# Kernel tuning notes

Measured on AMD Instinct MI355X. Metric: run time of the kernel, lower is better.

The kernel has to match this reference:

```python
import jax, jax.numpy as jnp
import numpy as np

L, N, C, OPL = 20, 512, 10, 13        # levels, nodes/level, conditions/node, condition op length
HID, MID = 512, 256                   # hidden_dim, hid_dim
OP_DIM, EX_DIM, SAMP_DIM = 15, 108, 1000
EPS = 1e-5


def _lstm_cell(x, h, c, wih, whh, bih, bhh):
    gates = x @ wih.T + h @ whh.T + bih + bhh
    i, f, g, o = jnp.split(gates, 4, axis=-1)  # torch gate order i,f,g,o
    c = jax.nn.sigmoid(f) * c + jax.nn.sigmoid(i) * jnp.tanh(g)
    h = jax.nn.sigmoid(o) * jnp.tanh(c)
    return h, c


def _batchnorm(x, g, b):  # training-mode BatchNorm1d (biased batch stats)
    m = x.mean(0)
    v = x.var(0)
    return (x - m) / jnp.sqrt(v + EPS) * g + b


def setup_inputs() -> dict:
    key = jax.random.key(0)
    ks = iter(jax.random.split(key, 48))
    rn = lambda shp, s=1.0: jax.random.normal(next(ks), shp, jnp.float32) * s
    ru = lambda shp: jax.random.uniform(next(ks), shp, jnp.float32)
    w = lambda shp: rn(shp, 0.05)
    inp = {
        'operators': ru((L, N, OP_DIM)),
        'extra_infos': rn((L, N, EX_DIM)),
        'condition1s': rn((L, N, C, OPL)),
        'condition2s': rn((L, N, C, OPL)),
        'samples': ru((L, N, SAMP_DIM)),
        'condition_masks': jnp.ones((L, N, 1), jnp.float32),
        'mapping': jax.random.randint(next(ks), (L, 2, N), 0, N + 1),
        # lstm1 (condition encoder)
        'w_ih1': w((4 * HID, OPL)), 'w_hh1': w((4 * HID, HID)),
        'b_ih1': w((4 * HID,)), 'b_hh1': w((4 * HID,)),
        # mlps feeding the tree lstm
        'sample_w': w((MID, SAMP_DIM)), 'sample_b': w((MID,)),
        'cond_w': w((MID, HID)), 'cond_b': w((MID,)),
        'bn1_g': jnp.ones((MID,), jnp.float32), 'bn1_b': jnp.zeros((MID,), jnp.float32),
        # lstm2 (tree aggregation)
        'w_ih2': w((4 * HID, OP_DIM + EX_DIM + 2 * MID)), 'w_hh2': w((4 * HID, HID)),
        'b_ih2': w((4 * HID,)), 'b_hh2': w((4 * HID,)),
        'bn2_g': jnp.ones((HID,), jnp.float32), 'bn2_b': jnp.zeros((HID,), jnp.float32),
        # task heads
        't1_w2': w((MID, HID)), 't1_b2': w((MID,)),
        't2_w2': w((MID, HID)), 't2_b2': w((MID,)),
        'bn3_g': jnp.ones((MID,), jnp.float32), 'bn3_b': jnp.zeros((MID,), jnp.float32),
        't1_w3': w((MID, MID)), 't1_b3': w((MID,)),
        't2_w3': w((MID, MID)), 't2_b3': w((MID,)),
        't1_ow': w((1, MID)), 't1_ob': w((1,)),
        't2_ow': w((1, MID)), 't2_ob': w((1,)),
    }
    return inp


def reference(operators, extra_infos, condition1s, condition2s, samples, condition_masks, mapping,
              w_ih1, w_hh1, b_ih1, b_hh1, sample_w, sample_b, cond_w, cond_b, bn1_g, bn1_b,
              w_ih2, w_hh2, b_ih2, b_hh2, bn2_g, bn2_b,
              t1_w2, t1_b2, t2_w2, t2_b2, bn3_g, bn3_b,
              t1_w3, t1_b3, t2_w3, t2_b3, t1_ow, t1_ob, t2_ow, t2_ob):
    Lv, Np = operators.shape[0], operators.shape[1]
    mapping = mapping.astype(jnp.int32)

    # --- condition encoder: lstm1 over each node's predicate sequence ---
    x = condition1s.reshape(Lv * Np, C, OPL)
    h0 = jnp.zeros((Lv * Np, HID), operators.dtype)

    def step1(carry, xt):
        h, c = carry
        h, c = _lstm_cell(xt, h, c, w_ih1, w_hh1, b_ih1, b_hh1)
        return (h, c), None

    (h_last, _), _ = jax.lax.scan(step1, (h0, h0), jnp.swapaxes(x, 0, 1))
    cond = _batchnorm(jax.nn.relu(h_last @ cond_w.T + cond_b), bn1_g, bn1_b)
    cond = cond.reshape(Lv, Np, MID)

    samp = jax.nn.relu(samples @ sample_w.T + sample_b) * condition_masks
    feats = jnp.concatenate([operators, extra_infos, cond, samp], axis=2)  # [L, N, 123+2*MID]

    # --- bottom level: lstm2 single step from zero state ---
    z0 = jnp.zeros((Np, HID), feats.dtype)
    hid, cid = _lstm_cell(feats[Lv - 1], z0, z0, w_ih2, w_hh2, b_ih2, b_hh2)

    # --- bottom-up tree aggregation: gather children states, average, lstm2 step ---
    def level_step(carry, inputs):
        hid, cid = carry
        x_lvl, mapp = inputs  # x_lvl [N, F], mapp [2, N], index 0 == pad (no child)
        pad = jnp.zeros((1, HID), hid.dtype)
        nh = jnp.concatenate([pad, hid], axis=0)  # [N+1, H]
        nc = jnp.concatenate([pad, cid], axis=0)
        h = (nh[mapp[0]] + nh[mapp[1]]) * 0.5
        c = (nc[mapp[0]] + nc[mapp[1]]) * 0.5
        hid, cid = _lstm_cell(x_lvl, h, c, w_ih2, w_hh2, b_ih2, b_hh2)
        return (hid, cid), None

    xs = (feats[Lv - 2::-1], mapping[Lv - 2::-1])
    (hid, cid), _ = jax.lax.scan(level_step, (hid, cid), xs)

    # --- heads (batch_size == Np: all level-0 nodes active for these inputs) ---
    z = _batchnorm(hid, bn2_g, bn2_b)
    t1 = _batchnorm(jax.nn.relu(z @ t1_w2.T + t1_b2), bn3_g, bn3_b)
    t1 = jax.nn.sigmoid(jax.nn.relu(t1 @ t1_w3.T + t1_b3) @ t1_ow.T + t1_ob)
    t2 = _batchnorm(jax.nn.relu(z @ t2_w2.T + t2_b2), bn3_g, bn3_b)
    t2 = jax.nn.sigmoid(jax.nn.relu(t2 @ t2_w3.T + t2_b3) @ t2_ow.T + t2_ob)
    return t1, t2
```

## Files before the change

kernel.cpp:

```cpp
#include <hip/hip_runtime.h>
#include <hip/hip_bf16.h>


typedef __bf16 bf16x8 __attribute__((ext_vector_type(8)));
typedef float f32x4 __attribute__((ext_vector_type(4)));

#define MROWS 10240
#define LDH1  552
#define L1_ROWS 48
#define L1_BLOCKS 214
#define SAMP_BASE 214
#define FEAT_BASE 374
#define FUSED_BLOCKS 414

#define PF_BIAS1   0
#define PF_BIAS2   2048
#define PF_CONDB   4096
#define PF_SAMPB   4352
#define PF_BCAT2   4608
#define PF_B3CAT   5120
#define PF_BN1G    5632
#define PF_BN1B    5888
#define PF_BN2G    6144
#define PF_BN2B    6656
#define PF_BN3G    7168
#define PF_BN3B    7424
#define PF_OW      7680
#define PF_OB      8192
#define PF_TOTAL   8194

__device__ __forceinline__ float fsig(float x) {
  return __builtin_amdgcn_rcpf(1.0f + __expf(-x));
}
__device__ __forceinline__ float ftanh(float x) {
  return fmaf(2.0f, __builtin_amdgcn_rcpf(1.0f + __expf(-2.0f * x)), -1.0f);
}
__device__ __forceinline__ bf16x8 bzero8() {
  bf16x8 z;
#pragma unroll
  for (int i = 0; i < 8; ++i) z[i] = (__bf16)0.0f;
  return z;
}
__device__ __forceinline__ float ld_in(const void* p, long i, int bf) {
  return bf ? (float)((const __bf16*)p)[i] : ((const float*)p)[i];
}

__global__ void detect_kernel(const unsigned* __restrict__ masks, int* __restrict__ flag) {
  if (blockIdx.x == 0 && threadIdx.x == 0)
    *flag = (masks[0] == 0x3F803F80u) ? 1 : 0;
}

__global__ void prep_kernel(const int* __restrict__ flagp,
    const void* w_ih1, const void* w_hh1, const void* b_ih1, const void* b_hh1,
    const void* w_ih2, const void* w_hh2, const void* b_ih2, const void* b_hh2,
    const void* t1_w2, const void* t2_w2, const void* t1_b2, const void* t2_b2,
    const void* cond_w, const void* cond_b, const void* sample_w, const void* sample_b,
    const void* bn1_g, const void* bn1_b, const void* bn2_g, const void* bn2_b,
    const void* bn3_g, const void* bn3_b,
    const void* t1_w3, const void* t1_b3, const void* t2_w3, const void* t2_b3,
    const void* t1_ow, const void* t1_ob, const void* t2_ow, const void* t2_ob,
    const void* masks,
    __bf16* __restrict__ w1s, __bf16* __restrict__ w2s,
    __bf16* __restrict__ wcat2, __bf16* __restrict__ cond_w_bf,
    __bf16* __restrict__ sample_w_bf, __bf16* __restrict__ w3cat_bf,
    float* __restrict__ mask_f, float* __restrict__ pf)
{
  const int bf = *flagp;
  const int S1 = 2048 * 544;
  const int S2 = 2048 * 1152;
  const int S3 = 512 * 512;
  const int S4 = 256 * 512;
  const int S5 = 256 * 1000;
  const int S6 = 512 * 256;
  const int S7 = 10240;
  const int total = S1 + S2 + S3 + S4 + S5 + S6 + S7 + PF_TOTAL;
  for (int idx = blockIdx.x * blockDim.x + threadIdx.x; idx < total;
       idx += gridDim.x * blockDim.x) {
    int i = idx;
    if (i < S1) {
      int e = i & 7, l = (i >> 3) & 63, g = (i >> 9) & 3;
      int grp = i >> 11;
      int kk = grp % 17, cgt = grp / 17;
      int colq = l & 15, quad = l >> 4;
      int row = g * 512 + cgt * 16 + colq;
      int k = kk * 32 + quad * 8 + e;
      float v = (k < 512) ? ld_in(w_hh1, (long)row * 512 + k, bf)
              : (k < 525) ? ld_in(w_ih1, (long)row * 13 + (k - 512), bf) : 0.0f;
      w1s[i] = (__bf16)v;
      continue;
    }
    i -= S1;
    if (i < S2) {
      int e = i & 7, l = (i >> 3) & 63, g = (i >> 9) & 3;
      int grp = i >> 11;
      int kk = grp % 36, jt = grp / 36;
      int colq = l & 15, quad = l >> 4;
      int row = g * 512 + jt * 16 + colq;
      int k = kk * 32 + quad * 8 + e;
      float v = (k < 635) ? ld_in(w_ih2, (long)row * 635 + k, bf)
              : (k < 640) ? 0.0f : ld_in(w_hh2, (long)row * 512 + (k - 640), bf);
      w2s[i] = (__bf16)v;
      continue;
    }
    i -= S2;
    if (i < S3) {
      int r = i >> 9, k = i & 511;
      wcat2[i] = (__bf16)((r < 256) ? ld_in(t1_w2, r * 512 + k, bf)
                                    : ld_in(t2_w2, (r - 256) * 512 + k, bf));
      continue;
    }
    i -= S3;
    if (i < S4) { cond_w_bf[i] = (__bf16)ld_in(cond_w, i, bf); continue; }
    i -= S4;
    if (i < S5) { sample_w_bf[i] = (__bf16)ld_in(sample_w, i, bf); continue; }
    i -= S5;
    if (i < S6) {
      int r = i >> 8, k = i & 255;
      w3cat_bf[i] = (__bf16)((r < 256) ? ld_in(t1_w3, r * 256 + k, bf)
                                       : ld_in(t2_w3, (r - 256) * 256 + k, bf));
      continue;
    }
    i -= S6;
    if (i < S7) { mask_f[i] = ld_in(masks, i, bf); continue; }
    i -= S7;
    {
      int j = i;
      float v;
      if      (j < 2048) v = ld_in(b_ih1, j, bf) + ld_in(b_hh1, j, bf);
      else if (j < 4096) v = ld_in(b_ih2, j - 2048, bf) + ld_in(b_hh2, j - 2048, bf);
      else if (j < 4352) v = ld_in(cond_b, j - 4096, bf);
      else if (j < 4608) v = ld_in(sample_b, j - 4352, bf);
      else if (j < 5120) { int k = j - 4608; v = (k < 256) ? ld_in(t1_b2, k, bf) : ld_in(t2_b2, k - 256, bf); }
      else if (j < 5632) { int k = j - 5120; v = (k < 256) ? ld_in(t1_b3, k, bf) : ld_in(t2_b3, k - 256, bf); }
      else if (j < 5888) v = ld_in(bn1_g, j - 5632, bf);
      else if (j < 6144) v = ld_in(bn1_b, j - 5888, bf);
      else if (j < 6656) v = ld_in(bn2_g, j - 6144, bf);
      else if (j < 7168) v = ld_in(bn2_b, j - 6656, bf);
      else if (j < 7424) v = ld_in(bn3_g, j - 7168, bf);
      else if (j < 7680) v = ld_in(bn3_b, j - 7424, bf);
      else if (j < 8192) { int k = j - 7680; v = (k < 256) ? ld_in(t1_ow, k, bf) : ld_in(t2_ow, k - 256, bf); }
      else v = (j == 8192) ? ld_in(t1_ob, 0, bf) : ld_in(t2_ob, 0, bf);
      pf[j] = v;
    }
  }
}

__global__ void conv_samples_kernel(const int* __restrict__ flagp,
                                    const void* __restrict__ samples,
                                    __bf16* __restrict__ dst)
{
  const int bf = *flagp;
  if (bf) return;
  for (long i = blockIdx.x * blockDim.x + threadIdx.x; i < 10240000L;
       i += (long)gridDim.x * blockDim.x)
    dst[i] = (__bf16)ld_in(samples, i, bf);
}

__global__ __launch_bounds__(1024, 4) void fused1_kernel(
    const int* __restrict__ flagp,
    const void* __restrict__ cond1,
    const __bf16* __restrict__ w1s,
    const float*  __restrict__ bias,
    __bf16* __restrict__ h_out,
    const void* __restrict__ samples_raw,
    const __bf16* __restrict__ samp_bf,
    const __bf16* __restrict__ sample_w_bf,
    const float* __restrict__ sampb,
    __bf16* __restrict__ samp_out,
    const float* __restrict__ mask,
    const void* __restrict__ ops,
    const void* __restrict__ extra,
    __bf16* __restrict__ Astage,
    const __bf16* __restrict__ cond_w_bf,
    const float* __restrict__ condb,
    float* __restrict__ condtmp,
    float* __restrict__ partial)
{
  const int bf = *flagp;
  const int tid = threadIdx.x;

  if (blockIdx.x < L1_BLOCKS) {
    __shared__ __attribute__((aligned(16))) __bf16 hbuf[2][L1_ROWS * LDH1];
    const int wave = tid >> 6;
    const int lane = tid & 63;
    const int colq = lane & 15;
    const int quad = lane >> 4;
    const int r0   = blockIdx.x * L1_ROWS;

    {
      bf16x8 z8 = bzero8();
      for (int i = tid * 8; i < 2 * L1_ROWS * LDH1; i += 1024 * 8)
        *(bf16x8*)&hbuf[0][i] = z8;
    }
    __syncthreads();
    if (tid < L1_ROWS * 8) {
      int row = tid >> 3, jj = tid & 7;
      int gr = r0 + row;
      if (gr < MROWS) {
        long base = (long)gr * 130;
        hbuf[0][row * LDH1 + 512 + jj] = (__bf16)ld_in(cond1, base + jj, bf);
        if (jj < 5) hbuf[0][row * LDH1 + 520 + jj] = (__bf16)ld_in(cond1, base + 8 + jj, bf);
      }
    }
    __syncthreads();

    float c_reg[2][3][4];
#pragma unroll
    for (int a = 0; a < 2; ++a)
#pragma unroll
      for (int b = 0; b < 3; ++b)
#pragma unroll
        for (int r = 0; r < 4; ++r) c_reg[a][b][r] = 0.0f;

    const int jbase = wave * 32;

    float bI[2], bF[2], bG[2], bO[2];
#pragma unroll
    for (int cg = 0; cg < 2; ++cg) {
      const int j = jbase + cg * 16 + colq;
      bI[cg] = bias[j];
      bF[cg] = bias[512 + j];
      bG[cg] = bias[1024 + j];
      bO[cg] = bias[1536 + j];
    }

#pragma unroll 1
    for (int t = 0; t < 10; ++t) {
      const __bf16* hcur = hbuf[t & 1];
      __bf16* hnxt = hbuf[(t + 1) & 1];
#pragma unroll
      for (int cg = 0; cg < 2; ++cg) {
        const int jc = jbase + cg * 16;
        f32x4 acc[3][4];
#pragma unroll
        for (int a = 0; a < 3; ++a)
#pragma unroll
          for (int g = 0; g < 4; ++g)
#pragma unroll
            for (int r = 0; r < 4; ++r) acc[a][g][r] = 0.0f;

        const __bf16* wp = w1s + ((size_t)(wave * 2 + cg) * 17 * 4 * 512) + (lane << 3);
#pragma unroll 1
        for (int kk = 0; kk < 17; ++kk) {
          const int kof = (kk << 5) + (quad << 3);
          bf16x8 af[3];
#pragma unroll
          for (int rt = 0; rt < 3; ++rt)
            af[rt] = *(const bf16x8*)&hcur[(rt * 16 + colq) * LDH1 + kof];
          bf16x8 bfr[4];
#pragma unroll
          for (int g = 0; g < 4; ++g)
            bfr[g] = *(const bf16x8*)&wp[(kk * 4 + g) << 9];
#pragma unroll
          for (int g = 0; g < 4; ++g)
#pragma unroll
            for (int rt = 0; rt < 3; ++rt)
              acc[rt][g] = __builtin_amdgcn_mfma_f32_16x16x32_bf16(af[rt], bfr[g], acc[rt][g], 0, 0, 0);
        }
#pragma unroll
        for (int rt = 0; rt < 3; ++rt)
#pragma unroll
          for (int r = 0; r < 4; ++r) {
            float c = fsig(acc[rt][1][r] + bF[cg]) * c_reg[cg][rt][r]
                    + fsig(acc[rt][0][r] + bI[cg]) * ftanh(acc[rt][2][r] + bG[cg]);
            c_reg[cg][rt][r] = c;
            float h = fsig(acc[rt][3][r] + bO[cg]) * ftanh(c);
            hnxt[(rt * 16 + quad * 4 + r) * LDH1 + jc + colq] = (__bf16)h;
          }
      }
      if (t < 9 && tid < L1_ROWS * 8) {
        int row = tid >> 3, jj = tid & 7;
        int gr = r0 + row;
        if (gr < MROWS) {
          long base = ((long)gr * 10 + (t + 1)) * 13;
          hnxt[row * LDH1 + 512 + jj] = (__bf16)ld_in(cond1, base + jj, bf);
          if (jj < 5) hnxt[row * LDH1 + 520 + jj] = (__bf16)ld_in(cond1, base + 8 + jj, bf);
        }
      }
      __syncthreads();
    }

    for (int i = tid; i < L1_ROWS * 64; i += 1024) {
      int row = i >> 6;
      int cb  = (i & 63) << 3;
      *(bf16x8*)&h_out[(size_t)(r0 + row) * 512 + cb] = *(const bf16x8*)&hbuf[0][row * LDH1 + cb];
    }

    {
      const int ct = wave;
      f32x4 cacc[3];
#pragma unroll
      for (int rt = 0; rt < 3; ++rt)
#pragma unroll
        for (int r = 0; r < 4; ++r) cacc[rt][r] = 0.0f;

      const __bf16* wb = cond_w_bf + (size_t)(ct * 16 + colq) * 512;
#pragma unroll 1
      for (int kk = 0; kk < 16; ++kk) {
        const int kof = (kk << 5) + (quad << 3);
        bf16x8 bfr = *(const bf16x8*)&wb[kof];
#pragma unroll
        for (int rt = 0; rt < 3; ++rt) {
          bf16x8 af = *(const bf16x8*)&hbuf[0][(rt * 16 + colq) * LDH1 + kof];
          cacc[rt] = __builtin_amdgcn_mfma_f32_16x16x32_bf16(af, bfr, cacc[rt], 0, 0, 0);
        }
      }
      const int col = ct * 16 + colq;
      const float bv = condb[col];
      float s1 = 0.0f, s2 = 0.0f;
#pragma unroll
      for (int rt = 0; rt < 3; ++rt)
#pragma unroll
        for (int r = 0; r < 4; ++r) {
          const int lrow = rt * 16 + quad * 4 + r;
          const int grow = r0 + lrow;
          float v = fmaxf(cacc[rt][r] + bv, 0.0f);
          if (grow < MROWS) {
            condtmp[(size_t)grow * 256 + col] = v;
            s1 += v;
            s2 += v * v;
          }
        }
      s1 += __shfl_xor(s1, 16); s2 += __shfl_xor(s2, 16);
      s1 += __shfl_xor(s1, 32); s2 += __shfl_xor(s2, 32);
      if (quad == 0) {
        partial[(size_t)(2 * blockIdx.x) * 256 + col]     = s1;
        partial[(size_t)(2 * blockIdx.x + 1) * 256 + col] = s2;
      }
    }
    return;
  }

  if (blockIdx.x < FEAT_BASE) {
    const __bf16* A = bf ? (const __bf16*)samples_raw : samp_bf;
    const int vb   = (blockIdx.x - SAMP_BASE) * 4 + (tid >> 8);
    const int bx   = vb & 3;
    const int by   = vb >> 2;
    const int t    = tid & 255;
    const int wave = t >> 6;
    const int lane = t & 63;
    const int colq = lane & 15;
    const int quad = lane >> 4;
    const int m0 = by * 64 + (wave >> 1) * 32;
    const int n0 = bx * 64 + (wave & 1) * 32;
    const int K = 1000;

    f32x4 acc[2][2];
#pragma unroll
    for (int a = 0; a < 2; ++a)
#pragma unroll
      for (int b = 0; b < 2; ++b)
#pragma unroll
        for (int r = 0; r < 4; ++r) acc[a][b][r] = 0.0f;

    for (int kk = 0; kk < 32; ++kk) {
      const int kof = (kk << 5) + (quad << 3);
      bf16x8 a0, a1, b0, b1;
      if (kof < K) {
        a0 = *(const bf16x8*)&A[(size_t)(m0 + colq) * 1000 + kof];
        a1 = *(const bf16x8*)&A[(size_t)(m0 + 16 + colq) * 1000 + kof];
        b0 = *(const bf16x8*)&sample_w_bf[(size_t)(n0 + colq) * 1000 + kof];
        b1 = *(const bf16x8*)&sample_w_bf[(size_t)(n0 + 16 + colq) * 1000 + kof];
      } else {
        a0 = bzero8(); a1 = a0; b0 = a0; b1 = a0;
      }
      acc[0][0] = __builtin_amdgcn_mfma_f32_16x16x32_bf16(a0, b0, acc[0][0], 0, 0, 0);
      acc[0][1] = __builtin_amdgcn_mfma_f32_16x16x32_bf16(a0, b1, acc[0][1], 0, 0, 0);
      acc[1][0] = __builtin_amdgcn_mfma_f32_16x16x32_bf16(a1, b0, acc[1][0], 0, 0, 0);
      acc[1][1] = __builtin_amdgcn_mfma_f32_16x16x32_bf16(a1, b1, acc[1][1], 0, 0, 0);
    }
#pragma unroll
    for (int ai = 0; ai < 2; ++ai)
#pragma unroll
      for (int bi = 0; bi < 2; ++bi) {
        const int col = n0 + bi * 16 + colq;
        const float bv = sampb[col];
#pragma unroll
        for (int r = 0; r < 4; ++r) {
          const int row = m0 + ai * 16 + quad * 4 + r;
          float v = fmaxf(acc[ai][bi][r] + bv, 0.0f) * mask[row];
          samp_out[(size_t)row * 640 + col] = (__bf16)v;
        }
      }
    return;
  }

  for (int idx = (blockIdx.x - FEAT_BASE) * 1024 + tid; idx < 10240 * 128;
       idx += 40 * 1024) {
    int m = idx >> 7, c = idx & 127;
    float v; int col;
    if (c < 15)       { v = ld_in(ops, (long)m * 15 + c, bf);            col = c; }
    else if (c < 123) { v = ld_in(extra, (long)m * 108 + (c - 15), bf);  col = c; }
    else              { v = 0.0f;                                        col = 512 + c; }
    Astage[(size_t)m * 640 + col] = (__bf16)v;
  }
}

template<int ACT, int OUTBF, int MASKED>
__global__ __launch_bounds__(256, 4) void gemm_kernel(
    const __bf16* __restrict__ A, int lda,
    const __bf16* __restrict__ W, int ldw,
    const float* __restrict__ bias,
    float* __restrict__ outf, __bf16* __restrict__ outb, int ldc,
    const float* __restrict__ mask, int K)
{
  const int tid  = threadIdx.x;
  const int wave = tid >> 6;
  const int lane = tid & 63;
  const int colq = lane & 15;
  const int quad = lane >> 4;
  const int m0 = blockIdx.y * 64 + (wave >> 1) * 32;
  const int n0 = blockIdx.x * 64 + (wave & 1) * 32;

  f32x4 acc[2][2];
#pragma unroll
  for (int a = 0; a < 2; ++a)
#pragma unroll
    for (int b = 0; b < 2; ++b)
#pragma unroll
      for (int r = 0; r < 4; ++r) acc[a][b][r] = 0.0f;

  const int nk = (K + 31) >> 5;
  for (int kk = 0; kk < nk; ++kk) {
    const int kof = (kk << 5) + (quad << 3);
    bf16x8 a0, a1, b0, b1;
    if (kof < K) {
      a0 = *(const bf16x8*)&A[(size_t)(m0 + colq) * lda + kof];
      a1 = *(const bf16x8*)&A[(size_t)(m0 + 16 + colq) * lda + kof];
      b0 = *(const bf16x8*)&W[(size_t)(n0 + colq) * ldw + kof];
      b1 = *(const bf16x8*)&W[(size_t)(n0 + 16 + colq) * ldw + kof];
    } else {
      a0 = bzero8(); a1 = a0; b0 = a0; b1 = a0;
    }
    acc[0][0] = __builtin_amdgcn_mfma_f32_16x16x32_bf16(a0, b0, acc[0][0], 0, 0, 0);
    acc[0][1] = __builtin_amdgcn_mfma_f32_16x16x32_bf16(a0, b1, acc[0][1], 0, 0, 0);
    acc[1][0] = __builtin_amdgcn_mfma_f32_16x16x32_bf16(a1, b0, acc[1][0], 0, 0, 0);
    acc[1][1] = __builtin_amdgcn_mfma_f32_16x16x32_bf16(a1, b1, acc[1][1], 0, 0, 0);
  }
#pragma unroll
  for (int ai = 0; ai < 2; ++ai)
#pragma unroll
    for (int bi = 0; bi < 2; ++bi) {
      const int col = n0 + bi * 16 + colq;
      const float bv = bias[col];
#pragma unroll
      for (int r = 0; r < 4; ++r) {
        const int row = m0 + ai * 16 + quad * 4 + r;
        float v = acc[ai][bi][r] + bv;
        if (ACT) v = fmaxf(v, 0.0f);
        if (MASKED) v *= mask[row];
        if (OUTBF) outb[(size_t)row * ldc + col] = (__bf16)v;
        else       outf[(size_t)row * ldc + col] = v;
      }
    }
}

__global__ __launch_bounds__(1024, 4) void treelvl_kernel(
    const __bf16* __restrict__ Alvl,
    const __bf16* __restrict__ w2s,
    const float* __restrict__ bias,
    const int* __restrict__ mapping,
    const __bf16* __restrict__ h_src, const float* __restrict__ c_src,
    __bf16* __restrict__ h_dst, float* __restrict__ c_dst,
    float* __restrict__ h_f32, int first, int last)
{
  __shared__ float red[3][16 * 256];
  const int tid  = threadIdx.x;
  const int wave = tid >> 6;
  const int lane = tid & 63;
  const int colq = lane & 15;
  const int quad = lane >> 4;
  const int wv   = wave & 3;
  const int kq   = wave >> 2;
  const int jt = blockIdx.x;
  const int mt = blockIdx.y;
  const int rowA = mt * 64 + wv * 16 + colq;

  const __bf16* wbase = w2s + (size_t)jt * 36 * 4 * 512 + (lane << 3);

  f32x4 acc[4];
#pragma unroll
  for (int g = 0; g < 4; ++g)
#pragma unroll
    for (int r = 0; r < 4; ++r) acc[g][r] = 0.0f;

  if (kq < 2) {
    const __bf16* arow = Alvl + (size_t)rowA * 640;
    const int kb = kq * 10;
#pragma unroll 2
    for (int ki = 0; ki < 10; ++ki) {
      const int kk = kb + ki;
      const int kof = (kk << 5) + (quad << 3);
      bf16x8 afr = *(const bf16x8*)&arow[kof];
      bf16x8 b0 = *(const bf16x8*)&wbase[(kk * 4 + 0) << 9];
      bf16x8 b1 = *(const bf16x8*)&wbase[(kk * 4 + 1) << 9];
      bf16x8 b2 = *(const bf16x8*)&wbase[(kk * 4 + 2) << 9];
      bf16x8 b3 = *(const bf16x8*)&wbase[(kk * 4 + 3) << 9];
      acc[0] = __builtin_amdgcn_mfma_f32_16x16x32_bf16(afr, b0, acc[0], 0, 0, 0);
      acc[1] = __builtin_amdgcn_mfma_f32_16x16x32_bf16(afr, b1, acc[1], 0, 0, 0);
      acc[2] = __builtin_amdgcn_mfma_f32_16x16x32_bf16(afr, b2, acc[2], 0, 0, 0);
      acc[3] = __builtin_amdgcn_mfma_f32_16x16x32_bf16(afr, b3, acc[3], 0, 0, 0);
    }
  } else {
    int i0 = 0, i1 = 0;
    if (!first) { i0 = mapping[rowA]; i1 = mapping[512 + rowA]; }
    const float s0 = (i0 > 0) ? 0.5f : 0.0f;
    const float s1 = (i1 > 0) ? 0.5f : 0.0f;
    const __bf16* h0p = h_src + (size_t)((i0 > 0 ? i0 : 1) - 1) * 512;
    const __bf16* h1p = h_src + (size_t)((i1 > 0 ? i1 : 1) - 1) * 512;
    const int kb = 20 + (kq - 2) * 8;
#pragma unroll 2
    for (int ki = 0; ki < 8; ++ki) {
      const int kk = kb + ki;
      const int kh = ((kk - 20) << 5) + (quad << 3);
      bf16x8 v0 = *(const bf16x8*)&h0p[kh];
      bf16x8 v1 = *(const bf16x8*)&h1p[kh];
      bf16x8 afr;
#pragma unroll
      for (int e = 0; e < 8; ++e)
        afr[e] = (__bf16)((float)v0[e] * s0 + (float)v1[e] * s1);
      bf16x8 b0 = *(const bf16x8*)&wbase[(kk * 4 + 0) << 9];
      bf16x8 b1 = *(const bf16x8*)&wbase[(kk * 4 + 1) << 9];
      bf16x8 b2 = *(const bf16x8*)&wbase[(kk * 4 + 2) << 9];
      bf16x8 b3 = *(const bf16x8*)&wbase[(kk * 4 + 3) << 9];
      acc[0] = __builtin_amdgcn_mfma_f32_16x16x32_bf16(afr, b0, acc[0], 0, 0, 0);
      acc[1] = __builtin_amdgcn_mfma_f32_16x16x32_bf16(afr, b1, acc[1], 0, 0, 0);
      acc[2] = __builtin_amdgcn_mfma_f32_16x16x32_bf16(afr, b2, acc[2], 0, 0, 0);
      acc[3] = __builtin_amdgcn_mfma_f32_16x16x32_bf16(afr, b3, acc[3], 0, 0, 0);
    }
  }

  if (kq > 0) {
    float* rp = red[kq - 1];
    const int base = wv * 64 + lane;
#pragma unroll
    for (int g = 0; g < 4; ++g)
#pragma unroll
      for (int r = 0; r < 4; ++r)
        rp[(g * 4 + r) * 256 + base] = acc[g][r];
  }
  __syncthreads();
  if (kq != 0) return;

  {
    const int base = wv * 64 + lane;
#pragma unroll
    for (int s = 0; s < 3; ++s) {
      const float* rp = red[s];
#pragma unroll
      for (int g = 0; g < 4; ++g)
#pragma unroll
        for (int r = 0; r < 4; ++r)
          acc[g][r] += rp[(g * 4 + r) * 256 + base];
    }
  }

  const int j = jt * 16 + colq;
  const float bi  = bias[j];
  const float bff = bias[512 + j];
  const float bg  = bias[1024 + j];
  const float bo  = bias[1536 + j];
#pragma unroll
  for (int r = 0; r < 4; ++r) {
    const int mrow = mt * 64 + wv * 16 + quad * 4 + r;
    float ci = 0.0f;
    if (!first) {
      int a0 = mapping[mrow], a1 = mapping[512 + mrow];
      if (a0 > 0) ci += c_src[(size_t)(a0 - 1) * 512 + j];
      if (a1 > 0) ci += c_src[(size_t)(a1 - 1) * 512 + j];
      ci *= 0.5f;
    }
    float c = fsig(acc[1][r] + bff) * ci + fsig(acc[0][r] + bi) * ftanh(acc[2][r] + bg);
    float h = fsig(acc[3][r] + bo) * ftanh(c);
    h_dst[(size_t)mrow * 512 + j] = (__bf16)h;
    c_dst[(size_t)mrow * 512 + j] = c;
    if (last) h_f32[(size_t)mrow * 512 + j] = h;
  }
}

__global__ void stats1_kernel(const float* __restrict__ in, int ld, int N,
                              int rows_per_blk, float* __restrict__ partial)
{
  int b = blockIdx.x;
  int r0 = b * rows_per_blk;
  for (int c = threadIdx.x; c < N; c += blockDim.x) {
    float s = 0.0f, sq = 0.0f;
    for (int r = 0; r < rows_per_blk; ++r) {
      float v = in[(size_t)(r0 + r) * ld + c];
      s += v; sq += v * v;
    }
    partial[(size_t)(2 * b) * N + c] = s;
    partial[(size_t)(2 * b + 1) * N + c] = sq;
  }
}

__global__ void stats2_kernel(const float* __restrict__ partial, int nb, int N,
                              float invM, float* __restrict__ stats)
{
  int c = blockIdx.x * blockDim.x + threadIdx.x;
  if (c >= N) return;
  float s = 0.0f, sq = 0.0f;
  for (int b = 0; b < nb; ++b) {
    s  += partial[(size_t)(2 * b) * N + c];
    sq += partial[(size_t)(2 * b + 1) * N + c];
  }
  float mean = s * invM;
  float var  = sq * invM - mean * mean;
  stats[c]     = mean;
  stats[N + c] = rsqrtf(fmaxf(var, 0.0f) + 1e-5f);
}

__global__ void norm_kernel(const float* __restrict__ in, int ldin,
                            const float* __restrict__ stats, int N, int cshift, int gmask,
                            const float* __restrict__ g, const float* __restrict__ b,
                            __bf16* __restrict__ outp, int ldc, int total)
{
  for (int idx = blockIdx.x * blockDim.x + threadIdx.x; idx < total;
       idx += gridDim.x * blockDim.x) {
    int row = idx >> cshift;
    int c = idx & (N - 1);
    float v = (in[(size_t)row * ldin + c] - stats[c]) * stats[N + c];
    int gi = c & gmask;
    v = v * g[gi] + b[gi];
    outp[(size_t)row * ldc + c] = (__bf16)v;
  }
}

__global__ void head_kernel(const int* __restrict__ flagp,
                            const __bf16* __restrict__ tmp3,
                            const float* __restrict__ pf,
                            void* __restrict__ outp)
{
  const int bf = *flagp;
  const int gw   = blockIdx.x * 4 + (threadIdx.x >> 6);
  const int lane = threadIdx.x & 63;
  const int which = gw >> 9;
  const int n     = gw & 511;
  const __bf16* row = tmp3 + (size_t)n * 512 + which * 256;
  const float* ow = pf + PF_OW + which * 256;
  float s = 0.0f;
#pragma unroll
  for (int i = 0; i < 4; ++i) {
    const int k = lane + 64 * i;
    s += (float)row[k] * ow[k];
  }
#pragma unroll
  for (int off = 32; off > 0; off >>= 1)
    s += __shfl_down(s, off);
  if (lane == 0) {
    float v = fsig(s + pf[PF_OB + which]);
    if (bf) ((__bf16*)outp)[gw] = (__bf16)v;
    else    ((float*)outp)[gw]  = v;
  }
}

extern "C" void kernel_launch(void* const* d_in, const int* in_sizes, int n_in,
                              void* d_out, int out_size, void* d_ws, size_t ws_size,
                              hipStream_t stream) {
  const void* operators       = d_in[0];
  const void* extra_infos     = d_in[1];
  const void* condition1s     = d_in[2];
  const void* samples         = d_in[4];
  const void* condition_masks = d_in[5];
  const int*  mapping         = (const int*)d_in[6];
  (void)in_sizes; (void)n_in; (void)out_size; (void)ws_size;

  char* ws = (char*)d_ws;
  size_t off = 0;
  auto alloc = [&](size_t bytes) -> void* {
    void* p = ws + off;
    off += (bytes + 255) & ~(size_t)255;
    return p;
  };
  int*    flag     = (int*)   alloc(256);
  __bf16* w1s      = (__bf16*)alloc((size_t)2048 * 544 * 2);
  __bf16* w2s      = (__bf16*)alloc((size_t)2048 * 1152 * 2);
  __bf16* wcat2    = (__bf16*)alloc(512 * 512 * 2);
  __bf16* cond_w_bf   = (__bf16*)alloc(256 * 512 * 2);
  __bf16* sample_w_bf = (__bf16*)alloc(256 * 1000 * 2);
  __bf16* w3cat_bf    = (__bf16*)alloc(512 * 256 * 2);
  float*  mask_f   = (float*) alloc(10240 * 4);
  float*  pf       = (float*) alloc(PF_TOTAL * 4);
  __bf16* samp_bf  = (__bf16*)alloc((size_t)10240 * 1000 * 2);
  __bf16* h_last   = (__bf16*)alloc((size_t)10272 * 512 * 2);
  float*  condtmp  = (float*) alloc((size_t)10240 * 256 * 4);
  __bf16* Astage   = (__bf16*)alloc((size_t)20 * 512 * 640 * 2);
  __bf16* hs0      = (__bf16*)alloc(512 * 512 * 2);
  __bf16* hs1      = (__bf16*)alloc(512 * 512 * 2);
  float*  cs0      = (float*) alloc(512 * 512 * 4);
  float*  cs1      = (float*) alloc(512 * 512 * 4);
  float*  h_f32    = (float*) alloc(512 * 512 * 4);
  __bf16* zbuf     = (__bf16*)alloc(512 * 512 * 2);
  float*  tmp1     = (float*) alloc(512 * 512 * 4);
  __bf16* tmp2     = (__bf16*)alloc(512 * 512 * 2);
  __bf16* tmp3     = (__bf16*)alloc(512 * 512 * 2);
  float*  partial  = (float*) alloc((size_t)214 * 2 * 256 * 4 + 8 * 2 * 512 * 4);
  float*  statsb   = (float*) alloc(2 * 512 * 4);

  detect_kernel<<<1, 64, 0, stream>>>((const unsigned*)condition_masks, flag);
  prep_kernel<<<4096, 256, 0, stream>>>(flag,
      d_in[7], d_in[8], d_in[9], d_in[10],
      d_in[17], d_in[18], d_in[19], d_in[20],
      d_in[23], d_in[25], d_in[24], d_in[26],
      d_in[13], d_in[14], d_in[11], d_in[12],
      d_in[15], d_in[16], d_in[21], d_in[22],
      d_in[27], d_in[28],
      d_in[29], d_in[30], d_in[31], d_in[32],
      d_in[33], d_in[34], d_in[35], d_in[36],
      condition_masks,
      w1s, w2s, wcat2, cond_w_bf, sample_w_bf, w3cat_bf, mask_f, pf);

  conv_samples_kernel<<<4096, 256, 0, stream>>>(flag, samples, samp_bf);

  fused1_kernel<<<FUSED_BLOCKS, 1024, 0, stream>>>(flag,
      condition1s, w1s, pf + PF_BIAS1, h_last,
      samples, samp_bf, sample_w_bf, pf + PF_SAMPB, Astage + 379, mask_f,
      operators, extra_infos, Astage,
      cond_w_bf, pf + PF_CONDB, condtmp, partial);

  stats2_kernel<<<1, 256, 0, stream>>>(partial, 214, 256, 1.0f / 10240.0f, statsb);
  norm_kernel<<<2560, 256, 0, stream>>>(condtmp, 256, statsb, 256, 8, 255,
      pf + PF_BN1G, pf + PF_BN1B, Astage + 123, 640, 10240 * 256);

  for (int lvl = 19; lvl >= 0; --lvl) {
    __bf16* hd = (lvl & 1) ? hs1 : hs0;
    float*  cd = (lvl & 1) ? cs1 : cs0;
    const __bf16* hsrc = (lvl & 1) ? hs0 : hs1;
    const float*  csrc = (lvl & 1) ? cs0 : cs1;
    treelvl_kernel<<<dim3(32,8), 1024, 0, stream>>>(
        Astage + (size_t)lvl * 512 * 640, w2s, pf + PF_BIAS2,
        mapping + lvl * 1024, hsrc, csrc, hd, cd, h_f32,
        (lvl == 19) ? 1 : 0, (lvl == 0) ? 1 : 0);
  }

  stats1_kernel<<<8, 256, 0, stream>>>(h_f32, 512, 512, 64, partial);
  stats2_kernel<<<2, 256, 0, stream>>>(partial, 8, 512, 1.0f / 512.0f, statsb);
  norm_kernel<<<256, 256, 0, stream>>>(h_f32, 512, statsb, 512, 9, 511,
      pf + PF_BN2G, pf + PF_BN2B, zbuf, 512, 512 * 512);

  gemm_kernel<1,0,0><<<dim3(8,8), 256, 0, stream>>>(zbuf, 512, wcat2, 512,
      pf + PF_BCAT2, tmp1, nullptr, 512, nullptr, 512);
  stats1_kernel<<<8, 256, 0, stream>>>(tmp1, 512, 512, 64, partial);
  stats2_kernel<<<2, 256, 0, stream>>>(partial, 8, 512, 1.0f / 512.0f, statsb);
  norm_kernel<<<256, 256, 0, stream>>>(tmp1, 512, statsb, 512, 9, 255,
      pf + PF_BN3G, pf + PF_BN3B, tmp2, 512, 512 * 512);

  gemm_kernel<1,1,0><<<dim3(4,8), 256, 0, stream>>>(tmp2, 512, w3cat_bf, 256,
      pf + PF_B3CAT, nullptr, tmp3, 512, nullptr, 256);
  gemm_kernel<1,1,0><<<dim3(4,8), 256, 0, stream>>>(tmp2 + 256, 512, w3cat_bf + 256 * 256, 256,
      pf + PF_B3CAT + 256, nullptr, tmp3 + 256, 512, nullptr, 256);

  head_kernel<<<256, 256, 0, stream>>>(flag, tmp3, pf, d_out);
}
```

Baseline: 922.0 us.

## Fuse sample fp32-to-bf16 conversion into GEMM, parallelize BN1 stats, merge W3 GEMMs

```diff
diff --git a/kernel.cpp b/kernel.cpp
--- a/kernel.cpp
+++ b/kernel.cpp
@@ -145,17 +145,6 @@
   }
 }
 
-__global__ void conv_samples_kernel(const int* __restrict__ flagp,
-                                    const void* __restrict__ samples,
-                                    __bf16* __restrict__ dst)
-{
-  const int bf = *flagp;
-  if (bf) return;
-  for (long i = blockIdx.x * blockDim.x + threadIdx.x; i < 10240000L;
-       i += (long)gridDim.x * blockDim.x)
-    dst[i] = (__bf16)ld_in(samples, i, bf);
-}
-
 __global__ __launch_bounds__(1024, 4) void fused1_kernel(
     const int* __restrict__ flagp,
     const void* __restrict__ cond1,
@@ -163,7 +152,6 @@
     const float*  __restrict__ bias,
     __bf16* __restrict__ h_out,
     const void* __restrict__ samples_raw,
-    const __bf16* __restrict__ samp_bf,
     const __bf16* __restrict__ sample_w_bf,
     const float* __restrict__ sampb,
     __bf16* __restrict__ samp_out,
@@ -332,7 +320,6 @@
   }
 
   if (blockIdx.x < FEAT_BASE) {
-    const __bf16* A = bf ? (const __bf16*)samples_raw : samp_bf;
     const int vb   = (blockIdx.x - SAMP_BASE) * 4 + (tid >> 8);
     const int bx   = vb & 3;
     const int by   = vb >> 2;
@@ -357,8 +344,20 @@
       const int kof = (kk << 5) + (quad << 3);
       bf16x8 a0, a1, b0, b1;
       if (kof < K) {
-        a0 = *(const bf16x8*)&A[(size_t)(m0 + colq) * 1000 + kof];
-        a1 = *(const bf16x8*)&A[(size_t)(m0 + 16 + colq) * 1000 + kof];
+        if (bf) {
+          const __bf16* A = (const __bf16*)samples_raw;
+          a0 = *(const bf16x8*)&A[(size_t)(m0 + colq) * 1000 + kof];
+          a1 = *(const bf16x8*)&A[(size_t)(m0 + 16 + colq) * 1000 + kof];
+        } else {
+          const float* Af = (const float*)samples_raw;
+          const float* p0 = &Af[(size_t)(m0 + colq) * 1000 + kof];
+          const float* p1 = &Af[(size_t)(m0 + 16 + colq) * 1000 + kof];
+#pragma unroll
+          for (int e = 0; e < 8; ++e) {
+            a0[e] = (__bf16)p0[e];
+            a1[e] = (__bf16)p1[e];
+          }
+        }
         b0 = *(const bf16x8*)&sample_w_bf[(size_t)(n0 + colq) * 1000 + kof];
         b1 = *(const bf16x8*)&sample_w_bf[(size_t)(n0 + 16 + colq) * 1000 + kof];
       } else {
@@ -393,6 +392,29 @@
     else if (c < 123) { v = ld_in(extra, (long)m * 108 + (c - 15), bf);  col = c; }
     else              { v = 0.0f;                                        col = 512 + c; }
     Astage[(size_t)m * 640 + col] = (__bf16)v;
+  }
+}
+
+__global__ void bn1stats2_kernel(const float* __restrict__ partial,
+                                 float* __restrict__ stats)
+{
+  const int col  = blockIdx.x * 4 + (threadIdx.x >> 6);
+  const int lane = threadIdx.x & 63;
+  float s = 0.0f, sq = 0.0f;
+  for (int b = lane; b < L1_BLOCKS; b += 64) {
+    s  += partial[(size_t)(2 * b) * 256 + col];
+    sq += partial[(size_t)(2 * b + 1) * 256 + col];
+  }
+#pragma unroll
+  for (int off = 32; off > 0; off >>= 1) {
+    s  += __shfl_down(s, off);
+    sq += __shfl_down(sq, off);
+  }
+  if (lane == 0) {
+    float mean = s * (1.0f / 10240.0f);
+    float var  = sq * (1.0f / 10240.0f) - mean * mean;
+    stats[col]       = mean;
+    stats[256 + col] = rsqrtf(fmaxf(var, 0.0f) + 1e-5f);
   }
 }
 
@@ -451,6 +473,63 @@
         if (MASKED) v *= mask[row];
         if (OUTBF) outb[(size_t)row * ldc + col] = (__bf16)v;
         else       outf[(size_t)row * ldc + col] = v;
+      }
+    }
+}
+
+__global__ __launch_bounds__(256, 4) void w3gemm_kernel(
+    const __bf16* __restrict__ tmp2,
+    const __bf16* __restrict__ w3cat,
+    const float* __restrict__ b3,
+    __bf16* __restrict__ tmp3)
+{
+  const int which = blockIdx.x >> 2;
+  const int bx    = blockIdx.x & 3;
+  const __bf16* A = tmp2 + which * 256;
+  const __bf16* W = w3cat + (size_t)which * 256 * 256;
+  const float* bias = b3 + which * 256;
+  __bf16* outb = tmp3 + which * 256;
+  const int K = 256, lda = 512, ldw = 256, ldc = 512;
+
+  const int tid  = threadIdx.x;
+  const int wave = tid >> 6;
+  const int lane = tid & 63;
+  const int colq = lane & 15;
+  const int quad = lane >> 4;
+  const int m0 = blockIdx.y * 64 + (wave >> 1) * 32;
+  const int n0 = bx * 64 + (wave & 1) * 32;
+
+  f32x4 acc[2][2];
+#pragma unroll
+  for (int a = 0; a < 2; ++a)
+#pragma unroll
+    for (int b = 0; b < 2; ++b)
+#pragma unroll
+      for (int r = 0; r < 4; ++r) acc[a][b][r] = 0.0f;
+
+  for (int kk = 0; kk < 8; ++kk) {
+    const int kof = (kk << 5) + (quad << 3);
+    bf16x8 a0 = *(const bf16x8*)&A[(size_t)(m0 + colq) * lda + kof];
+    bf16x8 a1 = *(const bf16x8*)&A[(size_t)(m0 + 16 + colq) * lda + kof];
+    bf16x8 b0 = *(const bf16x8*)&W[(size_t)(n0 + colq) * ldw + kof];
+    bf16x8 b1 = *(const bf16x8*)&W[(size_t)(n0 + 16 + colq) * ldw + kof];
+    acc[0][0] = __builtin_amdgcn_mfma_f32_16x16x32_bf16(a0, b0, acc[0][0], 0, 0, 0);
+    acc[0][1] = __builtin_amdgcn_mfma_f32_16x16x32_bf16(a0, b1, acc[0][1], 0, 0, 0);
+    acc[1][0] = __builtin_amdgcn_mfma_f32_16x16x32_bf16(a1, b0, acc[1][0], 0, 0, 0);
+    acc[1][1] = __builtin_amdgcn_mfma_f32_16x16x32_bf16(a1, b1, acc[1][1], 0, 0, 0);
+  }
+  (void)K;
+#pragma unroll
+  for (int ai = 0; ai < 2; ++ai)
+#pragma unroll
+    for (int bi = 0; bi < 2; ++bi) {
+      const int col = n0 + bi * 16 + colq;
+      const float bv = bias[col];
+#pragma unroll
+      for (int r = 0; r < 4; ++r) {
+        const int row = m0 + ai * 16 + quad * 4 + r;
+        float v = fmaxf(acc[ai][bi][r] + bv, 0.0f);
+        outb[(size_t)row * ldc + col] = (__bf16)v;
       }
     }
 }
@@ -681,7 +760,6 @@
   __bf16* w3cat_bf    = (__bf16*)alloc(512 * 256 * 2);
   float*  mask_f   = (float*) alloc(10240 * 4);
   float*  pf       = (float*) alloc(PF_TOTAL * 4);
-  __bf16* samp_bf  = (__bf16*)alloc((size_t)10240 * 1000 * 2);
   __bf16* h_last   = (__bf16*)alloc((size_t)10272 * 512 * 2);
   float*  condtmp  = (float*) alloc((size_t)10240 * 256 * 4);
   __bf16* Astage   = (__bf16*)alloc((size_t)20 * 512 * 640 * 2);
@@ -710,15 +788,13 @@
       condition_masks,
       w1s, w2s, wcat2, cond_w_bf, sample_w_bf, w3cat_bf, mask_f, pf);
 
-  conv_samples_kernel<<<4096, 256, 0, stream>>>(flag, samples, samp_bf);
-
   fused1_kernel<<<FUSED_BLOCKS, 1024, 0, stream>>>(flag,
       condition1s, w1s, pf + PF_BIAS1, h_last,
-      samples, samp_bf, sample_w_bf, pf + PF_SAMPB, Astage + 379, mask_f,
+      samples, sample_w_bf, pf + PF_SAMPB, Astage + 379, mask_f,
       operators, extra_infos, Astage,
       cond_w_bf, pf + PF_CONDB, condtmp, partial);
 
-  stats2_kernel<<<1, 256, 0, stream>>>(partial, 214, 256, 1.0f / 10240.0f, statsb);
+  bn1stats2_kernel<<<64, 256, 0, stream>>>(partial, statsb);
   norm_kernel<<<2560, 256, 0, stream>>>(condtmp, 256, statsb, 256, 8, 255,
       pf + PF_BN1G, pf + PF_BN1B, Astage + 123, 640, 10240 * 256);
 
@@ -745,10 +821,7 @@
   norm_kernel<<<256, 256, 0, stream>>>(tmp1, 512, statsb, 512, 9, 255,
       pf + PF_BN3G, pf + PF_BN3B, tmp2, 512, 512 * 512);
 
-  gemm_kernel<1,1,0><<<dim3(4,8), 256, 0, stream>>>(tmp2, 512, w3cat_bf, 256,
-      pf + PF_B3CAT, nullptr, tmp3, 512, nullptr, 256);
-  gemm_kernel<1,1,0><<<dim3(4,8), 256, 0, stream>>>(tmp2 + 256, 512, w3cat_bf + 256 * 256, 256,
-      pf + PF_B3CAT + 256, nullptr, tmp3 + 256, 512, nullptr, 256);
+  w3gemm_kernel<<<dim3(8,8), 256, 0, stream>>>(tmp2, w3cat_bf, pf + PF_B3CAT, tmp3);
 
   head_kernel<<<256, 256, 0, stream>>>(flag, tmp3, pf, d_out);
 }
```

Measured after the change: 901.9 us. 2.2% less time.
